# Optimization experiments

Measured on AMD Instinct MI355X. Metric: run time of the kernel, lower is better.

## Reference

```python
import jax, jax.numpy as jnp
import numpy as np

T, B, S = 32, 64, 64      # tgt_len, batch, src_len
E, H, V = 512, 1024, 32000  # embed, hidden, vocab
LE, NL = 32, 4            # lang embed size, num languages
SCALE = 0.02


def setup_inputs() -> dict:
    key = jax.random.key(0)
    ks = jax.random.split(key, 20)
    r = lambda k, shp: SCALE * jax.random.normal(k, shp, dtype=jnp.float32)
    return {
        "x": jax.random.randint(ks[0], (T, B), 0, V),
        "src_lengths": jax.random.randint(ks[1], (B,), 1, S + 1),
        "lang_idx": 0,
        "h0": jax.random.normal(ks[2], (1, B, H), dtype=jnp.float32),
        "c0": jax.random.normal(ks[3], (1, B, H), dtype=jnp.float32),
        "src_encodings": jax.random.normal(ks[4], (S, B, H), dtype=jnp.float32),
        "vocab_embed": r(ks[5], (V, E)),
        "lang_embed": r(ks[6], (NL, LE)),
        "W_wih": r(ks[7], (4 * H * E, LE)), "b_wih": r(ks[8], (4 * H * E,)),
        "W_whh": r(ks[9], (4 * H * H, LE)), "b_whh": r(ks[10], (4 * H * H,)),
        "W_bih": r(ks[11], (4 * H, LE)), "b_bih": r(ks[12], (4 * H,)),
        "W_bhh": r(ks[13], (4 * H, LE)), "b_bhh": r(ks[14], (4 * H,)),
        "c2h_W": r(ks[15], (H, 2 * H)), "c2h_b": r(ks[16], (H,)),
        "h2o_W": r(ks[17], (V, H)), "h2o_b": r(ks[18], (V,)),
    }


def reference(x, src_lengths, lang_idx, h0, c0, src_encodings,
              vocab_embed, lang_embed,
              W_wih, b_wih, W_whh, b_whh, W_bih, b_bih, W_bhh, b_bhh,
              c2h_W, c2h_b, h2o_W, h2o_b):
    hdim = c0.shape[-1]
    emb = vocab_embed[x]                       # (T,B,E)
    el = lang_embed[lang_idx]                  # (LE,)
    # hypernetwork generates the LSTM cell weights for this language
    w_ih = (W_wih @ el + b_wih).reshape(4 * hdim, -1)   # (4H,E)
    w_hh = (W_whh @ el + b_whh).reshape(4 * hdim, hdim)  # (4H,H)
    b_ih = W_bih @ el + b_bih                  # (4H,)
    b_hh = W_bhh @ el + b_bhh

    def step(carry, xt):
        h, c = carry
        gates = xt @ w_ih.T + h @ w_hh.T + b_ih + b_hh
        i, f, g, o = jnp.split(gates, 4, axis=-1)
        c = jax.nn.sigmoid(f) * c + jax.nn.sigmoid(i) * jnp.tanh(g)
        h = jax.nn.sigmoid(o) * jnp.tanh(c)
        return (h, c), h

    (hN, cN), rnn_out = jax.lax.scan(step, (h0[0], c0[0]), emb)  # rnn_out (T,B,H)

    # Luong dot attention with source-length masking
    scores = jnp.einsum('tbh,sbh->tbs', rnn_out, src_encodings)
    mask = jnp.arange(src_encodings.shape[0])[None, :] < src_lengths[:, None]  # (B,S)
    scores = jnp.where(mask[None], scores, jnp.float32(-1e30))
    attn = jax.nn.softmax(scores, axis=-1)
    context = jnp.einsum('tbs,sbh->tbh', attn, src_encodings)

    concat = jnp.concatenate([context, rnn_out], axis=-1)   # (T,B,2H)
    attn_hidden = jnp.tanh(concat @ c2h_W.T + c2h_b)         # (T,B,H)
    output = attn_hidden @ h2o_W.T + h2o_b                   # (T,B,V)
    return output, hN[None], cN[None]
```

## Files before the change

kernel.cpp:

```cpp
#include <hip/hip_runtime.h>
#include <math.h>

#define Tt 32
#define Bb 64
#define Ss 64
#define Ee 512
#define Hh 1024
#define Vv 32000
#define LEc 32
#define G4H 4096
#define Mm 2048

typedef __bf16 bf16x8 __attribute__((ext_vector_type(8)));
typedef float f32x4 __attribute__((ext_vector_type(4)));
typedef short short4v __attribute__((ext_vector_type(4)));

__device__ __forceinline__ short f2bf(float f){
  unsigned u = __builtin_bit_cast(unsigned, f);
  u += 0x7fffu + ((u >> 16) & 1u);
  return (short)(u >> 16);
}

__device__ __forceinline__ void gl_lds16(const short* g, short* l){
  __builtin_amdgcn_global_load_lds((const __attribute__((address_space(1))) void*)g,
                                   (__attribute__((address_space(3))) void*)l, 16, 0, 0);
}

__global__ __launch_bounds__(256) void k_hyper_w(
    const float* __restrict__ Wih, const float* __restrict__ bihv,
    const float* __restrict__ Whh, const float* __restrict__ bhhv,
    const float* __restrict__ lang_embed, const int* __restrict__ lang_idx,
    short* __restrict__ w_ih, short* __restrict__ w_hh)
{
  const long NIH = (long)G4H * Ee;
  const long NALL = NIH + (long)G4H * Hh;
  long r = (long)blockIdx.x * 256 + threadIdx.x;
  if (r >= NALL) return;
  const float4* el4 = (const float4*)(lang_embed + (size_t)lang_idx[0] * LEc);
  float4 e[8];
  #pragma unroll
  for (int j = 0; j < 8; j++) e[j] = el4[j];
  const float4* W4; float bb; short* outp;
  if (r < NIH){ W4 = (const float4*)(Wih + r * LEc); bb = bihv[r]; outp = w_ih + r; }
  else { long rr = r - NIH; W4 = (const float4*)(Whh + rr * LEc); bb = bhhv[rr]; outp = w_hh + rr; }
  float acc = bb;
  #pragma unroll
  for (int j = 0; j < 8; j++){
    float4 w = W4[j];
    acc += w.x*e[j].x + w.y*e[j].y + w.z*e[j].z + w.w*e[j].w;
  }
  *outp = f2bf(acc);
}

__global__ __launch_bounds__(256) void k_hyper_b(
    const float* __restrict__ Wbih, const float* __restrict__ bbih,
    const float* __restrict__ Wbhh, const float* __restrict__ bbhh,
    const float* __restrict__ lang_embed, const int* __restrict__ lang_idx,
    float* __restrict__ b_total)
{
  int u = blockIdx.x * 256 + threadIdx.x;
  if (u >= G4H) return;
  const float* el = lang_embed + (size_t)lang_idx[0] * LEc;
  float acc = bbih[u] + bbhh[u];
  #pragma unroll
  for (int j = 0; j < LEc; j++)
    acc += (Wbih[(size_t)u*LEc + j] + Wbhh[(size_t)u*LEc + j]) * el[j];
  b_total[u] = acc;
}

__global__ __launch_bounds__(256) void k_embed(
    const int* __restrict__ x, const float* __restrict__ vocab, short* __restrict__ emb)
{
  int tid = blockIdx.x * 256 + threadIdx.x;
  if (tid >= Mm * Ee / 4) return;
  int row = tid / (Ee / 4);
  int j4 = (tid % (Ee / 4)) * 4;
  int tok = x[row];
  float4 v = *(const float4*)(vocab + (size_t)tok * Ee + j4);
  short4v o = { f2bf(v.x), f2bf(v.y), f2bf(v.z), f2bf(v.w) };
  *(short4v*)(emb + (size_t)row * Ee + j4) = o;
}

__global__ __launch_bounds__(256) void k_f2bf(const float* __restrict__ in, short* __restrict__ out, long n4)
{
  long i = (long)blockIdx.x * 256 + threadIdx.x;
  if (i >= n4) return;
  float4 v = ((const float4*)in)[i];
  short4v o = { f2bf(v.x), f2bf(v.y), f2bf(v.z), f2bf(v.w) };
  ((short4v*)out)[i] = o;
}

template<int M, int N, int K, int MODE>
__global__ __launch_bounds__(256) void k_gemm(
    const short* __restrict__ A, const short* __restrict__ B,
    const float* __restrict__ bias, void* __restrict__ Cv)
{
  __shared__ short lA[4096];
  __shared__ short lB[4096];
  const int nwg = (M/128)*(N/128);
  int xcd = blockIdx.x & 7, pos = blockIdx.x >> 3;
  int wg = xcd * (nwg >> 3) + pos;
  const int MT = M/128;
  int mt = wg % MT;
  int nt = wg / MT;

  int t = threadIdx.x;
  int wave = t >> 6, lane = t & 63;
  int wm = wave >> 1, wn = wave & 1;
  int tr = t >> 2;
  int tc = (t & 3) * 8;

  const short* Agp = A + (size_t)(mt*128)*K;
  const short* Bgp = B + (size_t)(nt*128)*K;

  f32x4 acc[4][4];
  #pragma unroll
  for (int i = 0; i < 4; i++)
    #pragma unroll
    for (int j = 0; j < 4; j++) acc[i][j] = (f32x4){0.f,0.f,0.f,0.f};

  int ra = lane & 15, ko = (lane >> 4) * 8;

  for (int k0 = 0; k0 < K; k0 += 32){
    #pragma unroll
    for (int q2 = 0; q2 < 2; q2++){
      gl_lds16(Agp + (size_t)(q2*64 + tr)*K + k0 + tc, &lA[q2*2048 + wave*512]);
      gl_lds16(Bgp + (size_t)(q2*64 + tr)*K + k0 + tc, &lB[q2*2048 + wave*512]);
    }
    __syncthreads();
    bf16x8 av[4], bv[4];
    #pragma unroll
    for (int i = 0; i < 4; i++){
      av[i] = *(const bf16x8*)&lA[(wm*64 + i*16 + ra)*32 + ko];
      bv[i] = *(const bf16x8*)&lB[(wn*64 + i*16 + ra)*32 + ko];
    }
    #pragma unroll
    for (int i = 0; i < 4; i++)
      #pragma unroll
      for (int j = 0; j < 4; j++)
        acc[i][j] = __builtin_amdgcn_mfma_f32_16x16x32_bf16(av[i], bv[j], acc[i][j], 0, 0, 0);
    __syncthreads();
  }

  int col = lane & 15, r0 = (lane >> 4) * 4;
  #pragma unroll
  for (int i = 0; i < 4; i++)
    #pragma unroll
    for (int j = 0; j < 4; j++)
      #pragma unroll
      for (int q = 0; q < 4; q++){
        int m = mt*128 + wm*64 + i*16 + r0 + q;
        int n = nt*128 + wn*64 + j*16 + col;
        float v = acc[i][j][q] + bias[n];
        if (MODE == 0) ((float*)Cv)[(size_t)m * N + n] = v;
        else           ((short*)Cv)[(size_t)m * N + n] = f2bf(tanhf(v));
      }
}

__global__ __launch_bounds__(256) void k_init_hc(
    const float* __restrict__ h0, const float* __restrict__ c0,
    short* __restrict__ hbf, float* __restrict__ c)
{
  int i = blockIdx.x * 256 + threadIdx.x;
  if (i >= Bb * Hh) return;
  hbf[i] = f2bf(h0[i]);
  c[i] = c0[i];
}

__global__ __launch_bounds__(256) void k_step(
    int t, const short* __restrict__ h_in, const short* __restrict__ w_hh,
    const float* __restrict__ Gx, float* __restrict__ c,
    short* __restrict__ h_out, float* __restrict__ rnn_out, short* __restrict__ concat)
{
  __shared__ float red[4][4][16][16];
  int mt = blockIdx.x >> 6;
  int n0 = (blockIdx.x & 63) * 16;
  int wv = threadIdx.x >> 6;
  int lane = threadIdx.x & 63;
  int ra = lane & 15, ko = (lane >> 4) * 8;
  f32x4 acc[4] = {{0,0,0,0},{0,0,0,0},{0,0,0,0},{0,0,0,0}};
  const short* Ap = h_in + (size_t)(mt*16 + ra) * Hh + wv*256 + ko;
  const short* Bp = w_hh + (size_t)(n0    + ra) * Hh + wv*256 + ko;
  #pragma unroll
  for (int kk = 0; kk < 256; kk += 32){
    bf16x8 a = *(const bf16x8*)(Ap + kk);
    #pragma unroll
    for (int g = 0; g < 4; g++){
      bf16x8 b = *(const bf16x8*)(Bp + (size_t)g*Hh*Hh + kk);
      acc[g] = __builtin_amdgcn_mfma_f32_16x16x32_bf16(a, b, acc[g], 0, 0, 0);
    }
  }
  int col = lane & 15, r0 = (lane >> 4) * 4;
  #pragma unroll
  for (int g = 0; g < 4; g++)
    #pragma unroll
    for (int i = 0; i < 4; i++)
      red[wv][g][r0 + i][col] = acc[g][i];
  __syncthreads();

  int r  = threadIdx.x >> 4;
  int cc = threadIdx.x & 15;
  int b  = mt*16 + r;
  int u  = n0 + cc;
  float gate[4];
  #pragma unroll
  for (int g = 0; g < 4; g++){
    float s = Gx[((size_t)t*Bb + b) * G4H + g*Hh + u];
    #pragma unroll
    for (int w2 = 0; w2 < 4; w2++) s += red[w2][g][r][cc];
    gate[g] = s;
  }
  float ig = 1.f / (1.f + expf(-gate[0]));
  float fg = 1.f / (1.f + expf(-gate[1]));
  float gg = tanhf(gate[2]);
  float og = 1.f / (1.f + expf(-gate[3]));
  size_t bu = (size_t)b * Hh + u;
  float cn = fg * c[bu] + ig * gg;
  c[bu] = cn;
  float hn = og * tanhf(cn);
  h_out[bu] = f2bf(hn);
  size_t row = (size_t)t * Bb + b;
  rnn_out[row * Hh + u] = hn;
  concat[row * (2*Hh) + Hh + u] = f2bf(hn);
}

__global__ __launch_bounds__(64) void k_scores(
    const float* __restrict__ rnn_out, const float* __restrict__ src,
    const int* __restrict__ src_len, float* __restrict__ attn)
{
  int t = blockIdx.x >> 6;
  int b = blockIdx.x & 63;
  int s = threadIdx.x;
  const float4* rp = (const float4*)(rnn_out + ((size_t)t*Bb + b) * Hh);
  const float4* sp = (const float4*)(src     + ((size_t)s*Bb + b) * Hh);
  float acc = 0.f;
  #pragma unroll 4
  for (int i = 0; i < Hh/4; i++){
    float4 rv = rp[i], sv = sp[i];
    acc += rv.x*sv.x + rv.y*sv.y + rv.z*sv.z + rv.w*sv.w;
  }
  if (s >= src_len[b]) acc = -1e30f;
  float mx = acc;
  for (int o = 32; o; o >>= 1) mx = fmaxf(mx, __shfl_xor(mx, o, 64));
  float p = expf(acc - mx);
  float sum = p;
  for (int o = 32; o; o >>= 1) sum += __shfl_xor(sum, o, 64);
  attn[((size_t)t*Bb + b) * Ss + s] = p / sum;
}

__global__ __launch_bounds__(256) void k_context(
    const float* __restrict__ attn, const float* __restrict__ src, short* __restrict__ concat)
{
  __shared__ float sat[8][64];
  int b  = blockIdx.x & 63;
  int t0 = (blockIdx.x >> 6) * 8;
  int tid = threadIdx.x;
  for (int i = tid; i < 8*64; i += 256){
    int ti = i >> 6, s = i & 63;
    sat[ti][s] = attn[((size_t)(t0 + ti)*Bb + b) * Ss + s];
  }
  __syncthreads();
  int h0 = tid * 4;
  float4 acc[8];
  #pragma unroll
  for (int i = 0; i < 8; i++) acc[i] = make_float4(0.f, 0.f, 0.f, 0.f);
  for (int s = 0; s < Ss; s++){
    float4 sv = *(const float4*)(src + ((size_t)s*Bb + b) * Hh + h0);
    #pragma unroll
    for (int i = 0; i < 8; i++){
      float a = sat[i][s];
      acc[i].x += a*sv.x; acc[i].y += a*sv.y; acc[i].z += a*sv.z; acc[i].w += a*sv.w;
    }
  }
  #pragma unroll
  for (int i = 0; i < 8; i++){
    size_t row = (size_t)(t0 + i)*Bb + b;
    short4v o = { f2bf(acc[i].x), f2bf(acc[i].y), f2bf(acc[i].z), f2bf(acc[i].w) };
    *(short4v*)(concat + row * (2*Hh) + h0) = o;
  }
}

__global__ __launch_bounds__(256) void k_final(
    const float* __restrict__ rnn_out, const float* __restrict__ c, float* __restrict__ out)
{
  int i = blockIdx.x * 256 + threadIdx.x;
  if (i >= Bb * Hh) return;
  out[(size_t)Mm * Vv + i]           = rnn_out[(size_t)(Tt-1)*Bb*Hh + i];
  out[(size_t)Mm * Vv + Bb*Hh + i]   = c[i];
}

extern "C" void kernel_launch(void* const* d_in, const int* in_sizes, int n_in,
                              void* d_out, int out_size, void* d_ws, size_t ws_size,
                              hipStream_t stream) {
  const int*   x         = (const int*)  d_in[0];
  const int*   src_len   = (const int*)  d_in[1];
  const int*   lang_idx  = (const int*)  d_in[2];
  const float* h0        = (const float*)d_in[3];
  const float* c0        = (const float*)d_in[4];
  const float* src       = (const float*)d_in[5];
  const float* vocab     = (const float*)d_in[6];
  const float* lang_emb  = (const float*)d_in[7];
  const float* Wih       = (const float*)d_in[8];
  const float* bih       = (const float*)d_in[9];
  const float* Whh       = (const float*)d_in[10];
  const float* bhh       = (const float*)d_in[11];
  const float* Wbih      = (const float*)d_in[12];
  const float* bbih      = (const float*)d_in[13];
  const float* Wbhh      = (const float*)d_in[14];
  const float* bbhh      = (const float*)d_in[15];
  const float* c2hW      = (const float*)d_in[16];
  const float* c2hb      = (const float*)d_in[17];
  const float* h2oW      = (const float*)d_in[18];
  const float* h2ob      = (const float*)d_in[19];
  float* out = (float*)d_out;

  char* ws = (char*)d_ws;
  short* w_ih   = (short*)(ws + 0);
  short* w_hh   = (short*)(ws + 4194304);
  short* c2hWb  = (short*)(ws + 12582912);
  short* h2oWb  = (short*)(ws + 16777216);
  float* b_tot  = (float*)(ws + 82313216);
  short* emb    = (short*)(ws + 82329600);
  float* Gx     = (float*)(ws + 84426752);
  short* hb0    = (short*)(ws + 117981184);
  short* hb1    = (short*)(ws + 118112256);
  float* cbuf   = (float*)(ws + 118243328);
  float* rnn    = (float*)(ws + 118505472);
  short* concat = (short*)(ws + 126894080);
  float* attn   = (float*)(ws + 135282688);
  short* ah     = (short*)(ws + 135806976);

  k_hyper_w<<<24576, 256, 0, stream>>>(Wih, bih, Whh, bhh, lang_emb, lang_idx, w_ih, w_hh);
  k_hyper_b<<<16, 256, 0, stream>>>(Wbih, bbih, Wbhh, bbhh, lang_emb, lang_idx, b_tot);
  k_embed<<<1024, 256, 0, stream>>>(x, vocab, emb);
  k_f2bf<<<2048, 256, 0, stream>>>(c2hW, c2hWb, (long)Hh*2*Hh/4);
  k_f2bf<<<32000, 256, 0, stream>>>(h2oW, h2oWb, (long)Vv*Hh/4);
  k_init_hc<<<256, 256, 0, stream>>>(h0, c0, hb0, cbuf);

  k_gemm<Mm, G4H, Ee, 0><<<(Mm/128)*(G4H/128), 256, 0, stream>>>(emb, w_ih, b_tot, Gx);

  short* hbuf[2] = { hb0, hb1 };
  for (int t = 0; t < Tt; t++){
    k_step<<<256, 256, 0, stream>>>(t, hbuf[t & 1], w_hh, Gx, cbuf,
                                    hbuf[(t + 1) & 1], rnn, concat);
  }

  k_scores<<<Tt*Bb, 64, 0, stream>>>(rnn, src, src_len, attn);
  k_context<<<256, 256, 0, stream>>>(attn, src, concat);

  k_gemm<Mm, Hh, 2*Hh, 1><<<(Mm/128)*(Hh/128), 256, 0, stream>>>(concat, c2hWb, c2hb, ah);
  k_gemm<Mm, Vv, Hh, 0><<<(Mm/128)*(Vv/128), 256, 0, stream>>>(ah, h2oWb, h2ob, out);

  k_final<<<256, 256, 0, stream>>>(rnn, cbuf, out);
}
```

Measured before the change: 810.1 us.

## Fuse LSTM time steps into one persistent cooperative kernel with grid sync

```diff
diff --git a/kernel.cpp b/kernel.cpp
--- a/kernel.cpp
+++ b/kernel.cpp
@@ -1,5 +1,8 @@
 #include <hip/hip_runtime.h>
+#include <hip/hip_cooperative_groups.h>
 #include <math.h>
+
+namespace cg = cooperative_groups;
 
 #define Tt 32
 #define Bb 64
@@ -157,71 +160,82 @@
       }
 }
 
-__global__ __launch_bounds__(256) void k_init_hc(
-    const float* __restrict__ h0, const float* __restrict__ c0,
-    short* __restrict__ hbf, float* __restrict__ c)
+__global__ __launch_bounds__(256) void k_init_h(
+    const float* __restrict__ h0, short* __restrict__ hbf)
 {
   int i = blockIdx.x * 256 + threadIdx.x;
   if (i >= Bb * Hh) return;
   hbf[i] = f2bf(h0[i]);
-  c[i] = c0[i];
-}
-
-__global__ __launch_bounds__(256) void k_step(
-    int t, const short* __restrict__ h_in, const short* __restrict__ w_hh,
-    const float* __restrict__ Gx, float* __restrict__ c,
-    short* __restrict__ h_out, float* __restrict__ rnn_out, short* __restrict__ concat)
-{
+}
+
+__global__ __launch_bounds__(256) void k_scan(
+    const short* __restrict__ w_hh, const float* __restrict__ Gx,
+    const float* __restrict__ c0, short* __restrict__ hb0, short* __restrict__ hb1,
+    float* __restrict__ rnn_out, short* __restrict__ concat, float* __restrict__ out)
+{
+  cg::grid_group grid = cg::this_grid();
   __shared__ float red[4][4][16][16];
   int mt = blockIdx.x >> 6;
   int n0 = (blockIdx.x & 63) * 16;
   int wv = threadIdx.x >> 6;
   int lane = threadIdx.x & 63;
   int ra = lane & 15, ko = (lane >> 4) * 8;
-  f32x4 acc[4] = {{0,0,0,0},{0,0,0,0},{0,0,0,0},{0,0,0,0}};
-  const short* Ap = h_in + (size_t)(mt*16 + ra) * Hh + wv*256 + ko;
-  const short* Bp = w_hh + (size_t)(n0    + ra) * Hh + wv*256 + ko;
-  #pragma unroll
-  for (int kk = 0; kk < 256; kk += 32){
-    bf16x8 a = *(const bf16x8*)(Ap + kk);
-    #pragma unroll
-    for (int g = 0; g < 4; g++){
-      bf16x8 b = *(const bf16x8*)(Bp + (size_t)g*Hh*Hh + kk);
-      acc[g] = __builtin_amdgcn_mfma_f32_16x16x32_bf16(a, b, acc[g], 0, 0, 0);
-    }
-  }
-  int col = lane & 15, r0 = (lane >> 4) * 4;
-  #pragma unroll
-  for (int g = 0; g < 4; g++)
-    #pragma unroll
-    for (int i = 0; i < 4; i++)
-      red[wv][g][r0 + i][col] = acc[g][i];
-  __syncthreads();
+  int col = lane & 15, r0w = (lane >> 4) * 4;
 
   int r  = threadIdx.x >> 4;
   int cc = threadIdx.x & 15;
   int b  = mt*16 + r;
   int u  = n0 + cc;
-  float gate[4];
-  #pragma unroll
-  for (int g = 0; g < 4; g++){
-    float s = Gx[((size_t)t*Bb + b) * G4H + g*Hh + u];
-    #pragma unroll
-    for (int w2 = 0; w2 < 4; w2++) s += red[w2][g][r][cc];
-    gate[g] = s;
-  }
-  float ig = 1.f / (1.f + expf(-gate[0]));
-  float fg = 1.f / (1.f + expf(-gate[1]));
-  float gg = tanhf(gate[2]);
-  float og = 1.f / (1.f + expf(-gate[3]));
   size_t bu = (size_t)b * Hh + u;
-  float cn = fg * c[bu] + ig * gg;
-  c[bu] = cn;
-  float hn = og * tanhf(cn);
-  h_out[bu] = f2bf(hn);
-  size_t row = (size_t)t * Bb + b;
-  rnn_out[row * Hh + u] = hn;
-  concat[row * (2*Hh) + Hh + u] = f2bf(hn);
+  float c_reg = c0[bu];
+
+  short* hbuf[2] = { hb0, hb1 };
+
+  for (int t = 0; t < Tt; t++){
+    const short* h_in = hbuf[t & 1];
+    short*       h_out = hbuf[(t + 1) & 1];
+
+    f32x4 acc[4] = {{0,0,0,0},{0,0,0,0},{0,0,0,0},{0,0,0,0}};
+    const short* Ap = h_in + (size_t)(mt*16 + ra) * Hh + wv*256 + ko;
+    const short* Bp = w_hh + (size_t)(n0    + ra) * Hh + wv*256 + ko;
+    #pragma unroll
+    for (int kk = 0; kk < 256; kk += 32){
+      bf16x8 a = *(const bf16x8*)(Ap + kk);
+      #pragma unroll
+      for (int g = 0; g < 4; g++){
+        bf16x8 bv = *(const bf16x8*)(Bp + (size_t)g*Hh*Hh + kk);
+        acc[g] = __builtin_amdgcn_mfma_f32_16x16x32_bf16(a, bv, acc[g], 0, 0, 0);
+      }
+    }
+    #pragma unroll
+    for (int g = 0; g < 4; g++)
+      #pragma unroll
+      for (int i = 0; i < 4; i++)
+        red[wv][g][r0w + i][col] = acc[g][i];
+    __syncthreads();
+
+    float gate[4];
+    #pragma unroll
+    for (int g = 0; g < 4; g++){
+      float s = Gx[((size_t)t*Bb + b) * G4H + g*Hh + u];
+      #pragma unroll
+      for (int w2 = 0; w2 < 4; w2++) s += red[w2][g][r][cc];
+      gate[g] = s;
+    }
+    float ig = 1.f / (1.f + expf(-gate[0]));
+    float fg = 1.f / (1.f + expf(-gate[1]));
+    float gg = tanhf(gate[2]);
+    float og = 1.f / (1.f + expf(-gate[3]));
+    c_reg = fg * c_reg + ig * gg;
+    float hn = og * tanhf(c_reg);
+    h_out[bu] = f2bf(hn);
+    size_t row = (size_t)t * Bb + b;
+    rnn_out[row * Hh + u] = hn;
+    concat[row * (2*Hh) + Hh + u] = f2bf(hn);
+
+    grid.sync();
+  }
+  out[(size_t)Mm * Vv + (size_t)Bb * Hh + bu] = c_reg;
 }
 
 __global__ __launch_bounds__(64) void k_scores(
@@ -281,12 +295,11 @@
 }
 
 __global__ __launch_bounds__(256) void k_final(
-    const float* __restrict__ rnn_out, const float* __restrict__ c, float* __restrict__ out)
+    const float* __restrict__ rnn_out, float* __restrict__ out)
 {
   int i = blockIdx.x * 256 + threadIdx.x;
   if (i >= Bb * Hh) return;
-  out[(size_t)Mm * Vv + i]           = rnn_out[(size_t)(Tt-1)*Bb*Hh + i];
-  out[(size_t)Mm * Vv + Bb*Hh + i]   = c[i];
+  out[(size_t)Mm * Vv + i] = rnn_out[(size_t)(Tt-1)*Bb*Hh + i];
 }
 
 extern "C" void kernel_launch(void* const* d_in, const int* in_sizes, int n_in,
@@ -324,7 +337,6 @@
   float* Gx     = (float*)(ws + 84426752);
   short* hb0    = (short*)(ws + 117981184);
   short* hb1    = (short*)(ws + 118112256);
-  float* cbuf   = (float*)(ws + 118243328);
   float* rnn    = (float*)(ws + 118505472);
   short* concat = (short*)(ws + 126894080);
   float* attn   = (float*)(ws + 135282688);
@@ -335,14 +347,16 @@
   k_embed<<<1024, 256, 0, stream>>>(x, vocab, emb);
   k_f2bf<<<2048, 256, 0, stream>>>(c2hW, c2hWb, (long)Hh*2*Hh/4);
   k_f2bf<<<32000, 256, 0, stream>>>(h2oW, h2oWb, (long)Vv*Hh/4);
-  k_init_hc<<<256, 256, 0, stream>>>(h0, c0, hb0, cbuf);
+  k_init_h<<<256, 256, 0, stream>>>(h0, hb0);
 
   k_gemm<Mm, G4H, Ee, 0><<<(Mm/128)*(G4H/128), 256, 0, stream>>>(emb, w_ih, b_tot, Gx);
 
-  short* hbuf[2] = { hb0, hb1 };
-  for (int t = 0; t < Tt; t++){
-    k_step<<<256, 256, 0, stream>>>(t, hbuf[t & 1], w_hh, Gx, cbuf,
-                                    hbuf[(t + 1) & 1], rnn, concat);
+  {
+    const short* w_hh_a = w_hh; const float* Gx_a = Gx; const float* c0_a = c0;
+    short* hb0_a = hb0; short* hb1_a = hb1;
+    float* rnn_a = rnn; short* concat_a = concat; float* out_a = out;
+    void* args[] = { &w_hh_a, &Gx_a, &c0_a, &hb0_a, &hb1_a, &rnn_a, &concat_a, &out_a };
+    hipLaunchCooperativeKernel((void*)k_scan, dim3(256), dim3(256), args, 0, stream);
   }
 
   k_scores<<<Tt*Bb, 64, 0, stream>>>(rnn, src, src_len, attn);
@@ -351,5 +365,5 @@
   k_gemm<Mm, Hh, 2*Hh, 1><<<(Mm/128)*(Hh/128), 256, 0, stream>>>(concat, c2hWb, c2hb, ah);
   k_gemm<Mm, Vv, Hh, 0><<<(Mm/128)*(Vv/128), 256, 0, stream>>>(ah, h2oWb, h2ob, out);
 
-  k_final<<<256, 256, 0, stream>>>(rnn, cbuf, out);
-}
+  k_final<<<256, 256, 0, stream>>>(rnn, out);
+}
```

Measured after the change: 1.676 ms. +106.9%, slower.

## Replace h2o GEMM with 256x256-tile, 8-wave, double-buffered pipelined kernel

Applied to the files above, without the earlier changes.

```diff
diff --git a/kernel.cpp b/kernel.cpp
--- a/kernel.cpp
+++ b/kernel.cpp
@@ -154,6 +154,129 @@
         float v = acc[i][j][q] + bias[n];
         if (MODE == 0) ((float*)Cv)[(size_t)m * N + n] = v;
         else           ((short*)Cv)[(size_t)m * N + n] = f2bf(tanhf(v));
+      }
+}
+
+#define VMW4 asm volatile("s_waitcnt vmcnt(4)" ::: "memory")
+#define VMW0 asm volatile("s_waitcnt vmcnt(0)" ::: "memory")
+#define VMNONE ((void)0)
+
+#define PHASE(d, lp, LOADB, VMW, ...) do { \
+    bf16x8 afr[2][2]; \
+    _Pragma("unroll") \
+    for (int ii = 0; ii < 2; ii++){ \
+      _Pragma("unroll") \
+      for (int ks = 0; ks < 2; ks++){ \
+        int r = (2*(lp)+ii)*16 + la15; \
+        int sc = (ks*4 + l4) ^ (r & 7); \
+        afr[ii][ks] = *(const bf16x8*)(lds + ((d)*2+wm)*16384 + (r*8+sc)*16); \
+      } \
+    } \
+    if (LOADB){ \
+      _Pragma("unroll") \
+      for (int fj = 0; fj < 4; fj++){ \
+        _Pragma("unroll") \
+        for (int ks = 0; ks < 2; ks++){ \
+          int grow = wn*64 + fj*16 + la15; \
+          int hh = grow >> 7, rb = grow & 127; \
+          int sc = (ks*4 + l4) ^ (rb & 7); \
+          bfr[fj][ks] = *(const bf16x8*)(lds + 65536 + ((d)*2+hh)*16384 + (rb*8+sc)*16); \
+        } \
+      } \
+    } \
+    __VA_ARGS__; \
+    __builtin_amdgcn_s_barrier(); \
+    asm volatile("s_waitcnt lgkmcnt(0)" ::: "memory"); \
+    __builtin_amdgcn_sched_barrier(0); \
+    __builtin_amdgcn_s_setprio(1); \
+    _Pragma("unroll") \
+    for (int ii = 0; ii < 2; ii++){ \
+      _Pragma("unroll") \
+      for (int ks = 0; ks < 2; ks++){ \
+        _Pragma("unroll") \
+        for (int fj = 0; fj < 4; fj++){ \
+          acc[2*(lp)+ii][fj] = __builtin_amdgcn_mfma_f32_16x16x32_bf16(afr[ii][ks], bfr[fj][ks], acc[2*(lp)+ii][fj], 0, 0, 0); \
+        } \
+      } \
+    } \
+    __builtin_amdgcn_s_setprio(0); \
+    VMW; \
+    __builtin_amdgcn_s_barrier(); \
+  } while (0)
+
+__global__ __launch_bounds__(512, 2) void k_h2o8(
+    const short* __restrict__ A, const short* __restrict__ Bw,
+    const float* __restrict__ bias, float* __restrict__ C)
+{
+  extern __shared__ char lds[];
+  int xcd = blockIdx.x & 7, pos = blockIdx.x >> 3;
+  int wg = xcd * 125 + pos;
+  int mt = wg % 8;
+  int nt = wg / 8;
+
+  int tid = threadIdx.x;
+  int wave = tid >> 6, lane = tid & 63;
+  int wm = wave >> 2, wn = wave & 3;
+  int la15 = lane & 15, l4 = lane >> 4;
+
+  const short* Ag = A  + (size_t)(mt*256)*Hh;
+  const short* Bg = Bw + (size_t)(nt*256)*Hh;
+
+  auto stage_half = [&](const short* G, int Xoff, int d, int h, int kt){
+    #pragma unroll
+    for (int call = 0; call < 2; call++){
+      int chunk = call*512 + tid;
+      int rr = chunk >> 3;
+      int cc = (chunk & 7) ^ (rr & 7);
+      const short* src = G + (size_t)(h*128 + rr)*Hh + kt*64 + cc*8;
+      char* dst = lds + Xoff + (d*2+h)*16384 + call*8192 + wave*1024;
+      gl_lds16(src, (short*)dst);
+    }
+  };
+
+  f32x4 acc[8][4];
+  #pragma unroll
+  for (int i = 0; i < 8; i++)
+    #pragma unroll
+    for (int j = 0; j < 4; j++) acc[i][j] = (f32x4){0.f,0.f,0.f,0.f};
+  bf16x8 bfr[4][2];
+
+  stage_half(Ag, 0,     0, 0, 0); stage_half(Ag, 0,     0, 1, 0);
+  stage_half(Bg, 65536, 0, 0, 0); stage_half(Bg, 65536, 0, 1, 0);
+  stage_half(Bg, 65536, 1, 0, 1); stage_half(Bg, 65536, 1, 1, 1);
+  VMW4;
+  __builtin_amdgcn_s_barrier();
+
+  for (int it = 0; it < 7; it++){
+    int kt0 = 2*it;
+    PHASE(0, 0, true,  VMNONE, stage_half(Ag, 0,     1, 0, kt0+1));
+    PHASE(0, 1, false, VMNONE, stage_half(Ag, 0,     1, 1, kt0+1));
+    PHASE(0, 2, false, VMNONE, stage_half(Bg, 65536, 0, 0, kt0+2));
+    PHASE(0, 3, false, VMW4,   stage_half(Bg, 65536, 0, 1, kt0+2));
+    PHASE(1, 0, true,  VMNONE, stage_half(Ag, 0,     0, 0, kt0+2));
+    PHASE(1, 1, false, VMNONE, stage_half(Ag, 0,     0, 1, kt0+2));
+    PHASE(1, 2, false, VMNONE, stage_half(Bg, 65536, 1, 0, kt0+3));
+    PHASE(1, 3, false, VMW4,   stage_half(Bg, 65536, 1, 1, kt0+3));
+  }
+  PHASE(0, 0, true,  VMNONE, stage_half(Ag, 0, 1, 0, 15));
+  PHASE(0, 1, false, VMNONE, stage_half(Ag, 0, 1, 1, 15));
+  PHASE(0, 2, false, VMNONE, VMNONE);
+  PHASE(0, 3, false, VMW0,   VMNONE);
+  PHASE(1, 0, true,  VMNONE, VMNONE);
+  PHASE(1, 1, false, VMNONE, VMNONE);
+  PHASE(1, 2, false, VMNONE, VMNONE);
+  PHASE(1, 3, false, VMNONE, VMNONE);
+
+  int col = lane & 15, r0 = (lane >> 4) * 4;
+  #pragma unroll
+  for (int fi = 0; fi < 8; fi++)
+    #pragma unroll
+    for (int fj = 0; fj < 4; fj++)
+      #pragma unroll
+      for (int q = 0; q < 4; q++){
+        int m = mt*256 + wm*128 + fi*16 + r0 + q;
+        int n = nt*256 + wn*64 + fj*16 + col;
+        C[(size_t)m * Vv + n] = acc[fi][fj][q] + bias[n];
       }
 }
 
@@ -349,7 +472,8 @@
   k_context<<<256, 256, 0, stream>>>(attn, src, concat);
 
   k_gemm<Mm, Hh, 2*Hh, 1><<<(Mm/128)*(Hh/128), 256, 0, stream>>>(concat, c2hWb, c2hb, ah);
-  k_gemm<Mm, Vv, Hh, 0><<<(Mm/128)*(Vv/128), 256, 0, stream>>>(ah, h2oWb, h2ob, out);
+  hipFuncSetAttribute((const void*)k_h2o8, hipFuncAttributeMaxDynamicSharedMemorySize, 131072);
+  k_h2o8<<<1000, 512, 131072, stream>>>(ah, h2oWb, h2ob, out);
 
   k_final<<<256, 256, 0, stream>>>(rnn, cbuf, out);
 }
```

After: 777.7 us. 4.0% less time.
